# Performance work log

Measured on AMD Instinct MI355X. Metric: run time of the kernel, lower is better.

The kernel has to match this reference:

```python
import jax, jax.numpy as jnp
import numpy as np

N, D, H = 4096, 1024, 16
DK = D // H

def setup_inputs() -> dict:
    key = jax.random.key(0)
    k1, k2 = jax.random.split(key)
    X = jax.random.normal(k1, (N, D), dtype=jnp.float32)
    # torch nn.Linear(D, 2D, bias=False): weight [2D, D]; y = x @ W.T. Store as [D, 2D].
    Wqkv = jax.random.normal(k2, (D, 2 * D), dtype=jnp.float32) * (1.0 / np.sqrt(D))
    return {"X": X, "Wqkv": Wqkv}

def reference(X, Wqkv):
    n = X.shape[0]
    proj = X @ Wqkv                      # [N, 2D]
    qk, v = jnp.split(proj, 2, axis=-1)  # each [N, D]
    qk = qk.reshape(n, H, DK)
    v = v.reshape(n, H, DK)
    scale = DK ** 0.5
    scores = jnp.einsum('nhd,mhd->hnm', qk, qk) / scale  # [H, N, N], Q == K
    att = jax.nn.softmax(scores, axis=-1)
    out = jnp.einsum('hnm,mhd->nhd', att, v)              # [N, H, DK]
    return out.reshape(n, D)
```

## Files before the change

kernel.cpp:

```cpp
#include <hip/hip_runtime.h>

typedef unsigned short u16;
typedef unsigned int u32;
typedef __bf16 bf16x8 __attribute__((ext_vector_type(8)));
typedef float f32x4 __attribute__((ext_vector_type(4)));
typedef float f32x16 __attribute__((ext_vector_type(16)));
typedef int i32x2 __attribute__((ext_vector_type(2)));
typedef unsigned int u32x4 __attribute__((ext_vector_type(4)));

#define N_TOK 4096
#define DMODEL 1024
#define NH 16
#define DKH 64

__device__ inline u16 f2bf(float f){
  unsigned u = __float_as_uint(f);
  u += 0x7fffu + ((u >> 16) & 1u);
  return (u16)(u >> 16);
}

__device__ inline float fexp2(float x){ return __builtin_amdgcn_exp2f(x); }

__global__ __launch_bounds__(256) void k_convX(const float* __restrict__ X, u16* __restrict__ Xb){
  int i = blockIdx.x*256 + threadIdx.x;
  const float4 v = reinterpret_cast<const float4*>(X)[i];
  ushort4 o; o.x=f2bf(v.x); o.y=f2bf(v.y); o.z=f2bf(v.z); o.w=f2bf(v.w);
  reinterpret_cast<ushort4*>(Xb)[i] = o;
}

__global__ __launch_bounds__(256) void k_convW(const float* __restrict__ W, u16* __restrict__ Wt){
  __shared__ float tile[64][65];
  const int bn = blockIdx.x*64;
  const int bk = blockIdx.y*64;
  const int t = threadIdx.x;
  const int c4 = (t & 15)*4;
  const int r  = t >> 4;
  #pragma unroll
  for (int i=0;i<4;i++){
    int k = r + i*16;
    const float4 v = *reinterpret_cast<const float4*>(&W[(size_t)(bk+k)*2048 + bn + c4]);
    tile[k][c4+0]=v.x; tile[k][c4+1]=v.y; tile[k][c4+2]=v.z; tile[k][c4+3]=v.w;
  }
  __syncthreads();
  #pragma unroll
  for (int i=0;i<4;i++){
    int n = r + i*16;
    ushort4 o;
    o.x = f2bf(tile[c4+0][n]);
    o.y = f2bf(tile[c4+1][n]);
    o.z = f2bf(tile[c4+2][n]);
    o.w = f2bf(tile[c4+3][n]);
    *reinterpret_cast<ushort4*>(&Wt[(size_t)(bn+n)*1024 + bk + c4]) = o;
  }
}

__global__ __launch_bounds__(256) void k_gemm(const u16* __restrict__ A, const u16* __restrict__ B,
                                              u16* __restrict__ kf_g, u16* __restrict__ vf_g){
  __shared__ alignas(16) u16 As[128*64];
  __shared__ alignas(16) u16 Bs[128*64];
  const int bm = blockIdx.y*128, bn = blockIdx.x*128;
  const int tid = threadIdx.x, wid = tid>>6, lane = tid&63;
  const int wr = wid>>1, wc = wid&1;
  const int lr = lane&15, lg = lane>>4;
  f32x4 acc[4][4] = {};

  for (int kk=0; kk<DMODEL; kk+=64){
    __syncthreads();
    #pragma unroll
    for (int i=0;i<4;i++){
      const int chunk = (wid*4+i)*64 + lane;
      const int row = chunk>>3, koc = chunk&7;
      const int swz = koc ^ (row&7);
      const u16* ga = A + (size_t)(bm+row)*DMODEL + kk + swz*8;
      const u16* gb = B + (size_t)(bn+row)*DMODEL + kk + swz*8;
      __builtin_amdgcn_global_load_lds((const __attribute__((address_space(1))) void*)ga,
          (__attribute__((address_space(3))) void*)(&As[(size_t)chunk*8]), 16, 0, 0);
      __builtin_amdgcn_global_load_lds((const __attribute__((address_space(1))) void*)gb,
          (__attribute__((address_space(3))) void*)(&Bs[(size_t)chunk*8]), 16, 0, 0);
    }
    asm volatile("s_waitcnt vmcnt(0)" ::: "memory");
    __syncthreads();
    #pragma unroll
    for (int ks=0; ks<2; ks++){
      bf16x8 af[4], bfr[4];
      #pragma unroll
      for (int m=0;m<4;m++){
        const int row = wr*64+m*16+lr, cr = ks*4+lg;
        af[m] = *reinterpret_cast<const bf16x8*>(&As[(size_t)(row*8 + (cr ^ (row&7)))*8]);
      }
      #pragma unroll
      for (int n=0;n<4;n++){
        const int row = wc*64+n*16+lr, cr = ks*4+lg;
        bfr[n] = *reinterpret_cast<const bf16x8*>(&Bs[(size_t)(row*8 + (cr ^ (row&7)))*8]);
      }
      #pragma unroll
      for (int m=0;m<4;m++)
        #pragma unroll
        for (int n=0;n<4;n++)
          acc[m][n] = __builtin_amdgcn_mfma_f32_16x16x32_bf16(af[m], bfr[n], acc[m][n], 0,0,0);
    }
  }

  #pragma unroll
  for (int m=0;m<4;m++){
    const int row0 = bm + wr*64 + m*16 + lg*4;
    #pragma unroll
    for (int n=0;n<4;n++){
      const int c = bn + wc*64 + n*16 + lr;
      if (c < DMODEL){
        const int hh = c>>6, d = c&63;
        const size_t base = ((size_t)hh*512 + (size_t)(row0>>5)*4 + (d>>4))*512;
        #pragma unroll
        for (int r=0;r<4;r++){
          const int row = row0 + r;
          kf_g[base + (size_t)(((row&31) | (((d>>3)&1)<<5)))*8 + (d&7)] = f2bf(acc[m][n][r]);
        }
      } else {
        const int cc = c - DMODEL; const int hh = cc>>6, d = cc&63;
        const size_t base = (((size_t)hh*64 + (row0>>6))*8 + (d>>5)*4 + ((row0>>4)&3))*512
                          + (size_t)(((d&31) | (((row0>>3)&1)<<5)))*8 + (row0&7);
        ushort4 o;
        o.x = f2bf(acc[m][n][0]); o.y = f2bf(acc[m][n][1]);
        o.z = f2bf(acc[m][n][2]); o.w = f2bf(acc[m][n][3]);
        *reinterpret_cast<ushort4*>(&vf_g[base]) = o;
      }
    }
  }
}

__device__ inline bf16x8 scale_bf8(bf16x8 v, float s){
  u32x4 w = __builtin_bit_cast(u32x4, v);
  u32x4 r;
  #pragma unroll
  for (int i=0;i<4;i++){
    float lo = __uint_as_float(w[i] << 16) * s;
    float hi = __uint_as_float(w[i] & 0xffff0000u) * s;
    u32 p;
    asm("v_cvt_pk_bf16_f32 %0, %1, %2" : "=v"(p) : "v"(lo), "v"(hi));
    r[i] = p;
  }
  return __builtin_bit_cast(bf16x8, r);
}

__global__ __launch_bounds__(256,3) void k_attn(const u16* __restrict__ kf_g, const u16* __restrict__ vf_g,
                                                float* __restrict__ out){
  __shared__ alignas(16) u16 stg[2][8192];
  const int bid  = blockIdx.x;
  const int xcd  = bid & 7;
  const int slot = bid >> 3;
  const int h    = (xcd<<1) | (slot>>5);
  const int qt   = slot & 31;
  const int wid  = threadIdx.x >> 6;
  const int lane = threadIdx.x & 63;
  const int ql   = lane & 31;
  const int q0   = qt*128 + wid*32;
  const u16* __restrict__ Kfh = kf_g + (size_t)h*262144;
  const u16* __restrict__ Vfh = vf_g + (size_t)h*262144;
  const float SC = 0.18033688011112042f;

  bf16x8 qb[4];
  #pragma unroll
  for (int ds=0; ds<4; ds++){
    bf16x8 raw = *reinterpret_cast<const bf16x8*>(&Kfh[(size_t)((q0>>5)*4 + ds)*512 + lane*8]);
    qb[ds] = scale_bf8(raw, SC);
  }

  f32x16 o0 = {}, o1 = {};
  float lp = 0.f;

  auto stage = [&](int buf, int t){
    #pragma unroll
    for (int i=0; i<4; i++){
      const int c = wid*4 + i;
      const u16* src = (c < 8)
        ? Kfh + ((size_t)(t*8 + c))*512 + lane*8
        : Vfh + ((size_t)(t*8 + c - 8))*512 + lane*8;
      __builtin_amdgcn_global_load_lds((const __attribute__((address_space(1))) void*)src,
          (__attribute__((address_space(3))) void*)(&stg[buf][(size_t)c*512]), 16, 0, 0);
    }
  };

  stage(0, 0);
  int cur = 0;
  for (int t=0; t<64; ++t){
    asm volatile("s_waitcnt vmcnt(0)" ::: "memory");
    __syncthreads();
    if (t < 63) stage(cur^1, t+1);

    const u16* kb = &stg[cur][0];
    #pragma unroll
    for (int ss=0; ss<2; ++ss){
      bf16x8 kf0 = *reinterpret_cast<const bf16x8*>(&kb[(size_t)(ss*4+0)*512 + lane*8]);
      bf16x8 kf1 = *reinterpret_cast<const bf16x8*>(&kb[(size_t)(ss*4+1)*512 + lane*8]);
      bf16x8 kf2 = *reinterpret_cast<const bf16x8*>(&kb[(size_t)(ss*4+2)*512 + lane*8]);
      bf16x8 kf3 = *reinterpret_cast<const bf16x8*>(&kb[(size_t)(ss*4+3)*512 + lane*8]);

      f32x16 p = {};
      p = __builtin_amdgcn_mfma_f32_32x32x16_bf16(kf0, qb[0], p, 0,0,0);
      p = __builtin_amdgcn_mfma_f32_32x32x16_bf16(kf1, qb[1], p, 0,0,0);
      p = __builtin_amdgcn_mfma_f32_32x32x16_bf16(kf2, qb[2], p, 0,0,0);
      p = __builtin_amdgcn_mfma_f32_32x32x16_bf16(kf3, qb[3], p, 0,0,0);

      const int vbase = (8 + ss*2)*512;
      bf16x8 va0 = *reinterpret_cast<const bf16x8*>(&kb[(size_t)vbase          + lane*8]);
      bf16x8 va1 = *reinterpret_cast<const bf16x8*>(&kb[(size_t)vbase +   512  + lane*8]);
      bf16x8 vb0 = *reinterpret_cast<const bf16x8*>(&kb[(size_t)vbase + 4*512  + lane*8]);
      bf16x8 vb1 = *reinterpret_cast<const bf16x8*>(&kb[(size_t)vbase + 5*512  + lane*8]);

      #pragma unroll
      for (int c=0; c<16; c++) p[c] = fexp2(p[c]);
      {
        float r0 = ((p[0]+p[1])+(p[2]+p[3])) + ((p[4]+p[5])+(p[6]+p[7]));
        float r1 = ((p[8]+p[9])+(p[10]+p[11])) + ((p[12]+p[13])+(p[14]+p[15]));
        lp += r0+r1;
      }

      u32 pk[8];
      #pragma unroll
      for (int c2=0; c2<8; c2++){
        u32 a;
        asm("v_cvt_pk_bf16_f32 %0, %1, %2" : "=v"(a) : "v"(p[2*c2]), "v"(p[2*c2+1]));
        pk[c2] = a;
      }
      #pragma unroll
      for (int t2=0; t2<2; t2++){
        const int base = 4*t2;
        i32x2 r0s = __builtin_amdgcn_permlane32_swap((int)pk[base+0], (int)pk[base+2], false, false);
        i32x2 r1s = __builtin_amdgcn_permlane32_swap((int)pk[base+1], (int)pk[base+3], false, false);
        u32x4 w; w[0] = (u32)r0s[0]; w[1] = (u32)r1s[0]; w[2] = (u32)r0s[1]; w[3] = (u32)r1s[1];
        bf16x8 bt = __builtin_bit_cast(bf16x8, w);
        o0 = __builtin_amdgcn_mfma_f32_32x32x16_bf16(t2 ? va1 : va0, bt, o0, 0,0,0);
        o1 = __builtin_amdgcn_mfma_f32_32x32x16_bf16(t2 ? vb1 : vb0, bt, o1, 0,0,0);
      }
    }
    __syncthreads();
    cur ^= 1;
  }

  lp += __shfl_xor(lp, 32, 64);

  const int hi = lane >> 5;
  const float inv = 1.f / lp;
  float* orow = out + (size_t)(q0 + ql)*DMODEL + h*DKH;
  #pragma unroll
  for (int g=0; g<4; g++){
    float4 s0, s1;
    s0.x = o0[4*g+0]*inv; s0.y = o0[4*g+1]*inv; s0.z = o0[4*g+2]*inv; s0.w = o0[4*g+3]*inv;
    s1.x = o1[4*g+0]*inv; s1.y = o1[4*g+1]*inv; s1.z = o1[4*g+2]*inv; s1.w = o1[4*g+3]*inv;
    *reinterpret_cast<float4*>(&orow[      8*g + 4*hi]) = s0;
    *reinterpret_cast<float4*>(&orow[32 +  8*g + 4*hi]) = s1;
  }
}

extern "C" void kernel_launch(void* const* d_in, const int* in_sizes, int n_in,
                              void* d_out, int out_size, void* d_ws, size_t ws_size,
                              hipStream_t stream) {
  const float* X = (const float*)d_in[0];
  const float* W = (const float*)d_in[1];
  float* out = (float*)d_out;
  u16* Xb = (u16*)d_ws;
  u16* Wt = Xb + (size_t)N_TOK*DMODEL;
  u16* Kf = Wt + (size_t)2*DMODEL*DMODEL;
  u16* Vf = Kf + (size_t)N_TOK*DMODEL;

  k_convX<<<dim3(4096), dim3(256), 0, stream>>>(X, Xb);
  k_convW<<<dim3(32,16), dim3(256), 0, stream>>>(W, Wt);
  k_gemm <<<dim3(16,32), dim3(256), 0, stream>>>(Xb, Wt, Kf, Vf);
  k_attn <<<dim3(512), dim3(256), 0, stream>>>(Kf, Vf, out);
}
```

Measured before the change: 119.6 us.

## Split attention key range across two wave groups per block and merge via LDS

```diff
diff --git a/kernel.cpp b/kernel.cpp
--- a/kernel.cpp
+++ b/kernel.cpp
@@ -142,9 +142,9 @@
   return __builtin_bit_cast(bf16x8, r);
 }
 
-__global__ __launch_bounds__(256,3) void k_attn(const u16* __restrict__ kf_g, const u16* __restrict__ vf_g,
+__global__ __launch_bounds__(512,2) void k_attn(const u16* __restrict__ kf_g, const u16* __restrict__ vf_g,
                                                 float* __restrict__ out){
-  __shared__ alignas(16) u16 stg[2][8192];
+  __shared__ alignas(16) u16 stg[2][2][8192];
   const int bid  = blockIdx.x;
   const int xcd  = bid & 7;
   const int slot = bid >> 3;
@@ -152,8 +152,10 @@
   const int qt   = slot & 31;
   const int wid  = threadIdx.x >> 6;
   const int lane = threadIdx.x & 63;
+  const int qw   = wid & 3;
+  const int kh   = wid >> 2;
   const int ql   = lane & 31;
-  const int q0   = qt*128 + wid*32;
+  const int q0   = qt*128 + qw*32;
   const u16* __restrict__ Kfh = kf_g + (size_t)h*262144;
   const u16* __restrict__ Vfh = vf_g + (size_t)h*262144;
   const float SC = 0.18033688011112042f;
@@ -171,23 +173,23 @@
   auto stage = [&](int buf, int t){
     #pragma unroll
     for (int i=0; i<4; i++){
-      const int c = wid*4 + i;
+      const int c = qw*4 + i;
       const u16* src = (c < 8)
-        ? Kfh + ((size_t)(t*8 + c))*512 + lane*8
-        : Vfh + ((size_t)(t*8 + c - 8))*512 + lane*8;
+        ? Kfh + ((size_t)(kh*256 + t*8 + c))*512 + lane*8
+        : Vfh + ((size_t)((kh*32 + t)*8 + c - 8))*512 + lane*8;
       __builtin_amdgcn_global_load_lds((const __attribute__((address_space(1))) void*)src,
-          (__attribute__((address_space(3))) void*)(&stg[buf][(size_t)c*512]), 16, 0, 0);
+          (__attribute__((address_space(3))) void*)(&stg[kh][buf][(size_t)c*512]), 16, 0, 0);
     }
   };
 
   stage(0, 0);
   int cur = 0;
-  for (int t=0; t<64; ++t){
+  for (int t=0; t<32; ++t){
     asm volatile("s_waitcnt vmcnt(0)" ::: "memory");
     __syncthreads();
-    if (t < 63) stage(cur^1, t+1);
-
-    const u16* kb = &stg[cur][0];
+    if (t < 31) stage(cur^1, t+1);
+
+    const u16* kb = &stg[kh][cur][0];
     #pragma unroll
     for (int ss=0; ss<2; ++ss){
       bf16x8 kf0 = *reinterpret_cast<const bf16x8*>(&kb[(size_t)(ss*4+0)*512 + lane*8]);
@@ -239,16 +241,31 @@
 
   lp += __shfl_xor(lp, 32, 64);
 
-  const int hi = lane >> 5;
-  const float inv = 1.f / lp;
-  float* orow = out + (size_t)(q0 + ql)*DMODEL + h*DKH;
-  #pragma unroll
-  for (int g=0; g<4; g++){
-    float4 s0, s1;
-    s0.x = o0[4*g+0]*inv; s0.y = o0[4*g+1]*inv; s0.z = o0[4*g+2]*inv; s0.w = o0[4*g+3]*inv;
-    s1.x = o1[4*g+0]*inv; s1.y = o1[4*g+1]*inv; s1.z = o1[4*g+2]*inv; s1.w = o1[4*g+3]*inv;
-    *reinterpret_cast<float4*>(&orow[      8*g + 4*hi]) = s0;
-    *reinterpret_cast<float4*>(&orow[32 +  8*g + 4*hi]) = s1;
+  float* cb = reinterpret_cast<float*>(&stg[0][0][0]);
+  if (kh){
+    float* c = &cb[(size_t)((qw<<6) | lane)*34];
+    #pragma unroll
+    for (int g=0; g<16; g++){ c[g] = o0[g]; c[16+g] = o1[g]; }
+    c[32] = lp;
+  }
+  __syncthreads();
+  if (!kh){
+    const float* c = &cb[(size_t)((qw<<6) | lane)*34];
+    #pragma unroll
+    for (int g=0; g<16; g++){ o0[g] += c[g]; o1[g] += c[16+g]; }
+    lp += c[32];
+
+    const int hi = lane >> 5;
+    const float inv = 1.f / lp;
+    float* orow = out + (size_t)(q0 + ql)*DMODEL + h*DKH;
+    #pragma unroll
+    for (int g=0; g<4; g++){
+      float4 s0, s1;
+      s0.x = o0[4*g+0]*inv; s0.y = o0[4*g+1]*inv; s0.z = o0[4*g+2]*inv; s0.w = o0[4*g+3]*inv;
+      s1.x = o1[4*g+0]*inv; s1.y = o1[4*g+1]*inv; s1.z = o1[4*g+2]*inv; s1.w = o1[4*g+3]*inv;
+      *reinterpret_cast<float4*>(&orow[      8*g + 4*hi]) = s0;
+      *reinterpret_cast<float4*>(&orow[32 +  8*g + 4*hi]) = s1;
+    }
   }
 }
 
@@ -266,5 +283,5 @@
   k_convX<<<dim3(4096), dim3(256), 0, stream>>>(X, Xb);
   k_convW<<<dim3(32,16), dim3(256), 0, stream>>>(W, Wt);
   k_gemm <<<dim3(16,32), dim3(256), 0, stream>>>(Xb, Wt, Kf, Vf);
-  k_attn <<<dim3(512), dim3(256), 0, stream>>>(Kf, Vf, out);
-}
+  k_attn <<<dim3(512), dim3(512), 0, stream>>>(Kf, Vf, out);
+}
```

After: 118.4 us. No clear change (-1.0%).
